# Optimization experiments

Hardware: AMD Instinct MI355X
Metric: run time of the kernel (lower is better)

Reference implementation:

```python
import jax, jax.numpy as jnp
import numpy as np

N, H, CIN, C, G = 50000, 16, 256, 256, 8
CPG = C // G          # 32 channels per group
CR = C // 4           # delta MLP hidden (delta_reduction=4)

def _lrelu(x):
    return jax.nn.leaky_relu(x, 0.1)

def setup_inputs() -> dict:
    key = jax.random.key(0)
    ks = jax.random.split(key, 16)
    def lin(k, fin, fout):
        return jax.random.normal(k, (fin, fout), jnp.float32) / np.sqrt(fin)
    return {
        'q_pts': jax.random.normal(ks[0], (N, 3), jnp.float32),
        's_pts': jax.random.normal(ks[1], (N, 3), jnp.float32),
        's_feats': jax.random.normal(ks[2], (N, CIN), jnp.float32),
        'neighb_inds': jax.random.randint(ks[3], (N, H), 0, N, jnp.int64),
        'Wq': lin(ks[4], CIN, C), 'bq': jnp.zeros((C,), jnp.float32),
        'Wk': lin(ks[5], CIN, C), 'bk': jnp.zeros((C,), jnp.float32),
        'Wv': lin(ks[6], CIN, C), 'bv': jnp.zeros((C,), jnp.float32),
        'Wd1': lin(ks[7], 3, CR), 'bd1': jnp.zeros((CR,), jnp.float32),
        'Wd2': lin(ks[8], CR, C), 'bd2': jnp.zeros((C,), jnp.float32),
        'Wa1': lin(ks[9], C, CPG), 'ba1': jnp.zeros((CPG,), jnp.float32),
        'Wa2': lin(ks[10], CPG, CPG), 'ba2': jnp.zeros((CPG,), jnp.float32),
    }

def reference(q_pts, s_pts, s_feats, neighb_inds,
              Wq, bq, Wk, bk, Wv, bv,
              Wd1, bd1, Wd2, bd2, Wa1, ba1, Wa2, ba2):
    # q/k/v projections  (N, C)
    v = s_feats @ Wv + bv
    k = s_feats @ Wk + bk
    q = s_feats @ Wq + bq
    # gather neighbor features (all indices < N, shadow mask is a no-op)
    nv = v[neighb_inds]                 # (N, H, C)
    nk = k[neighb_inds]                 # (N, H, C)
    # relative positions (torch.no_grad in source)
    rel = s_pts[neighb_inds] - q_pts[:, None, :]   # (N, H, 3)
    # delta MLP: 3 -> C/4 -> C (UnaryBlock + Linear, norm='none')
    geom = _lrelu(rel @ Wd1 + bd1) @ Wd2 + bd2     # (N, H, C)
    # geom_mode='sub': v-branch and qk-branch both subtract geom encodings
    nv = nv - geom
    # source always enters strided branch (s_pts padded before the check);
    # stride_mode='nearest' -> q feature of the first neighbor
    qf = q[neighb_inds[:, 0]]                      # (N, C)
    qk = qf[:, None, :] - nk - geom                # (N, H, C)
    # alpha MLP: NormBlock(id) + act, Linear C->CpG + act, Linear CpG->CpG
    a = _lrelu(qk)
    a = _lrelu(a @ Wa1 + ba1)
    a = a @ Wa2 + ba2                              # (N, H, CpG)
    attn = jax.nn.softmax(a, axis=1)               # softmax over neighbors
    # grouped weighted aggregation: C split as (CpG, G), attn broadcast over G
    out = (nv.reshape(N, H, CPG, G) * attn[..., None]).sum(axis=1)
    return out.reshape(N, C)
```

## Files before the change

kernel.cpp:

```cpp
#include <hip/hip_runtime.h>
#include <cstdint>
#include <cstddef>

#define N_PTS 50000
#define H 16
#define CIN 256
#define C 256
#define CPG 32
#define CR 64

typedef short bf16x8 __attribute__((ext_vector_type(8)));
typedef float f32x4 __attribute__((ext_vector_type(4)));

__device__ __forceinline__ unsigned short f2bf(float f) {
    unsigned int u = __float_as_uint(f);
    u += 0x7fff + ((u >> 16) & 1);
    return (unsigned short)(u >> 16);
}
__device__ __forceinline__ float bf2f(unsigned short s) {
    return __uint_as_float(((unsigned int)s) << 16);
}

__global__ __launch_bounds__(256) void prep_all(
    const float* __restrict__ feats,
    const float* __restrict__ Wq, const float* __restrict__ Wk,
    const float* __restrict__ Wv,
    const float* __restrict__ Wd2, const float* __restrict__ Wa1,
    const float* __restrict__ Wa2,
    unsigned short* __restrict__ A_bf16,
    unsigned short* __restrict__ gemmFrags,
    unsigned short* __restrict__ attnFrags)
{
    int bid = blockIdx.x;
    if (bid < 6250) {
        size_t i = ((size_t)bid * 256 + threadIdx.x) * 8;
        float4 f0 = *(const float4*)&feats[i];
        float4 f1 = *(const float4*)&feats[i + 4];
        unsigned short t[8] = {f2bf(f0.x), f2bf(f0.y), f2bf(f0.z), f2bf(f0.w),
                               f2bf(f1.x), f2bf(f1.y), f2bf(f1.z), f2bf(f1.w)};
        *(bf16x8*)&A_bf16[i] = *(bf16x8*)t;
    } else if (bid < 6346) {
        int t = (bid - 6250) * 256 + threadIdx.x;
        int lane = t & 63;
        int f = t >> 6;
        int ntg = f % 48;
        const float* W = ntg < 16 ? Wq : (ntg < 32 ? Wk : Wv);
        int colc = (ntg & 15) * 16 + (lane & 15);
        int row0 = (f / 48) * 32 + ((lane >> 4) << 3);
        unsigned short tmp[8];
        #pragma unroll
        for (int j = 0; j < 8; ++j) tmp[j] = f2bf(W[(size_t)(row0 + j) * 256 + colc]);
        *(bf16x8*)&gemmFrags[(size_t)t * 8] = *(bf16x8*)tmp;
    } else {
        int t = (bid - 6346) * 256 + threadIdx.x;
        if (t >= 3200) return;
        const float* W; int Nc, NT, loc, base;
        if (t < 2048)      { W = Wd2; Nc = 256; NT = 16; loc = t;        base = 0; }
        else if (t < 3072) { W = Wa1; Nc = 32;  NT = 2;  loc = t - 2048; base = 16384; }
        else               { W = Wa2; Nc = 32;  NT = 2;  loc = t - 3072; base = 24576; }
        int f = loc >> 6, lane = loc & 63;
        int kt = f / NT, nt = f - kt * NT;
        int colc = nt * 16 + (lane & 15);
        int row0 = kt * 32 + ((lane >> 4) << 3);
        unsigned short tmp[8];
        #pragma unroll
        for (int j = 0; j < 8; ++j) tmp[j] = f2bf(W[(size_t)(row0 + j) * Nc + colc]);
        *(bf16x8*)&attnFrags[(size_t)(base + loc * 8)] = *(bf16x8*)tmp;
    }
}

__global__ __launch_bounds__(256) void qkv_gemm_mfma(
    const unsigned short* __restrict__ A,
    const unsigned short* __restrict__ wfrags,
    const float* __restrict__ bq, const float* __restrict__ bk,
    const float* __restrict__ bv, unsigned short* __restrict__ out)
{
    const int tid = threadIdx.x;
    const int lane = tid & 63, wave = tid >> 6;
    const int quad = lane >> 4, col16 = lane & 15;
    const int bx = blockIdx.x, by = blockIdx.y;

    int r0 = by * 128 + wave * 32 + col16;
    int r1 = r0 + 16;
    r0 = r0 < N_PTS ? r0 : N_PTS - 1;
    r1 = r1 < N_PTS ? r1 : N_PTS - 1;
    const unsigned short* a0p = &A[(size_t)r0 * 256 + quad * 8];
    const unsigned short* a1p = &A[(size_t)r1 * 256 + quad * 8];
    const unsigned short* bp  = &wfrags[(((size_t)bx * 8) * 64 + lane) * 8];

    f32x4 acc[2][8] = {};

    #pragma unroll 2
    for (int kt = 0; kt < 8; ++kt) {
        bf16x8 af0 = *(const bf16x8*)(a0p + kt * 32);
        bf16x8 af1 = *(const bf16x8*)(a1p + kt * 32);
        const unsigned short* bkt = bp + (size_t)kt * 48 * 64 * 8;
        #pragma unroll
        for (int nt = 0; nt < 8; ++nt) {
            bf16x8 bf = *(const bf16x8*)(bkt + (size_t)nt * 64 * 8);
            acc[0][nt] = __builtin_amdgcn_mfma_f32_16x16x32_bf16(af0, bf, acc[0][nt], 0, 0, 0);
            acc[1][nt] = __builtin_amdgcn_mfma_f32_16x16x32_bf16(af1, bf, acc[1][nt], 0, 0, 0);
        }
    }

    const int mode = bx >> 1;
    const float* bias = mode == 0 ? bq : (mode == 1 ? bk : bv);
    #pragma unroll
    for (int nt = 0; nt < 8; ++nt) {
        int cIn = (bx & 1) * 128 + nt * 16 + col16;
        float bb = bias[cIn];
        int pos = mode == 0 ? cIn : (256 + 2 * cIn + (mode == 2 ? 1 : 0));
        #pragma unroll
        for (int mt = 0; mt < 2; ++mt) {
            #pragma unroll
            for (int r = 0; r < 4; ++r) {
                int row = by * 128 + wave * 32 + mt * 16 + quad * 4 + r;
                if (row < N_PTS)
                    out[(size_t)row * 768 + pos] = f2bf(acc[mt][nt][r] + bb);
            }
        }
    }
}

#define D1S 72
#define PGS 66
#define QKS 264
#define A1S 40
#define A2S 33

__global__ __launch_bounds__(256) void attn_mfma(
    const unsigned short* __restrict__ qkv,
    const float* __restrict__ q_pts, const float* __restrict__ s_pts,
    const int* __restrict__ nbr,
    const float* __restrict__ Wd1, const float* __restrict__ bd1,
    const float* __restrict__ bd2,
    const unsigned short* __restrict__ frags,
    const float* __restrict__ ba1, const float* __restrict__ ba2,
    float* __restrict__ out)
{
    __shared__ unsigned short s_d1[H * D1S];
    __shared__ float          s_pg[4 * H * PGS];
    __shared__ unsigned short s_qk[H * QKS];
    __shared__ unsigned short s_a1[H * A1S];
    __shared__ float          s_a2[H * A2S];
    __shared__ float          s_rel[4][H][3];
    __shared__ int            s_idx[4][H];

    const int tid = threadIdx.x;
    const int lane = tid & 63, wave = tid >> 6;
    const int quad = lane >> 4, col = lane & 15;
    const int n0 = blockIdx.x * 4;
    const int c = tid;

    if (tid < 64) {
        int pp = tid >> 4, hh = tid & 15;
        int idx = nbr[(size_t)(n0 + pp) * H + hh];
        s_idx[pp][hh] = idx;
        #pragma unroll
        for (int x = 0; x < 3; ++x)
            s_rel[pp][hh][x] = s_pts[(size_t)idx * 3 + x] - q_pts[(size_t)(n0 + pp) * 3 + x];
    }

    const float w1x = Wd1[lane], w1y = Wd1[64 + lane], w1z = Wd1[128 + lane];
    const float b1 = bd1[lane];
    const float b2 = bd2[c];
    bf16x8 wd2f[2][4];
    #pragma unroll
    for (int t = 0; t < 4; ++t) {
        wd2f[0][t] = *(const bf16x8*)&frags[((size_t)((0 * 16 + wave * 4 + t) * 64 + lane)) * 8];
        wd2f[1][t] = *(const bf16x8*)&frags[((size_t)((1 * 16 + wave * 4 + t) * 64 + lane)) * 8];
    }
    bf16x8 wa1f[8];
    bf16x8 wa2f = {0,0,0,0,0,0,0,0};
    if (wave < 2) {
        #pragma unroll
        for (int kt = 0; kt < 8; ++kt)
            wa1f[kt] = *(const bf16x8*)&frags[16384 + ((size_t)((kt * 2 + wave) * 64 + lane)) * 8];
        wa2f = *(const bf16x8*)&frags[24576 + ((size_t)(wave * 64 + lane)) * 8];
    }
    __syncthreads();

    float* pg = &s_pg[wave * (H * PGS)];

    for (int p = 0; p < 4; ++p) {
        const int n = n0 + p;

        #pragma unroll
        for (int pass = 0; pass < 4; ++pass) {
            int h = pass * 4 + wave;
            float v = b1 + s_rel[p][h][0] * w1x + s_rel[p][h][1] * w1y + s_rel[p][h][2] * w1z;
            s_d1[h * D1S + lane] = f2bf(fmaxf(v, 0.1f * v));
        }
        __syncthreads();

        unsigned int u[H];
        #pragma unroll
        for (int h = 0; h < H; ++h)
            u[h] = *(const unsigned int*)&qkv[(size_t)s_idx[p][h] * 768 + 256 + 2 * c];
        float qf = bf2f(qkv[(size_t)s_idx[p][0] * 768 + c]);

        {
            bf16x8 ga = *(bf16x8*)&s_d1[col * D1S + quad * 8];
            bf16x8 gb = *(bf16x8*)&s_d1[col * D1S + 32 + quad * 8];
            #pragma unroll
            for (int t = 0; t < 4; ++t) {
                f32x4 acc = {0.f, 0.f, 0.f, 0.f};
                acc = __builtin_amdgcn_mfma_f32_16x16x32_bf16(ga, wd2f[0][t], acc, 0, 0, 0);
                acc = __builtin_amdgcn_mfma_f32_16x16x32_bf16(gb, wd2f[1][t], acc, 0, 0, 0);
                #pragma unroll
                for (int rr = 0; rr < 4; ++rr)
                    pg[(quad * 4 + rr) * PGS + t * 16 + col] = acc[rr];
            }
        }

        float vg[H];
        #pragma unroll
        for (int h = 0; h < H; ++h) {
            float g = pg[h * PGS + lane] + b2;
            float nk = __uint_as_float(u[h] << 16);
            float nv = __uint_as_float(u[h] & 0xffff0000u);
            vg[h] = nv - g;
            float tq = qf - nk - g;
            s_qk[h * QKS + c] = f2bf(fmaxf(tq, 0.1f * tq));
        }
        __syncthreads();

        if (wave < 2) {
            f32x4 acc = {0.f, 0.f, 0.f, 0.f};
            #pragma unroll
            for (int kt = 0; kt < 8; ++kt) {
                bf16x8 a = *(bf16x8*)&s_qk[col * QKS + kt * 32 + quad * 8];
                acc = __builtin_amdgcn_mfma_f32_16x16x32_bf16(a, wa1f[kt], acc, 0, 0, 0);
            }
            int j = wave * 16 + col;
            float bb = ba1[j];
            #pragma unroll
            for (int rr = 0; rr < 4; ++rr) {
                float v = acc[rr] + bb;
                s_a1[(quad * 4 + rr) * A1S + j] = f2bf(fmaxf(v, 0.1f * v));
            }
        }
        __syncthreads();

        if (wave < 2) {
            bf16x8 aa = *(bf16x8*)&s_a1[col * A1S + quad * 8];
            f32x4 acc = {0.f, 0.f, 0.f, 0.f};
            acc = __builtin_amdgcn_mfma_f32_16x16x32_bf16(aa, wa2f, acc, 0, 0, 0);
            int j = wave * 16 + col;
            float bb = ba2[j];
            #pragma unroll
            for (int rr = 0; rr < 4; ++rr)
                s_a2[(quad * 4 + rr) * A2S + j] = acc[rr] + bb;
        }
        __syncthreads();

        if (wave == 0) {
            int j = lane & 31, hb = (lane >> 5) * 8;
            float vals[8];
            float mx = -1e30f;
            #pragma unroll
            for (int i = 0; i < 8; ++i) {
                vals[i] = s_a2[(hb + i) * A2S + j];
                mx = fmaxf(mx, vals[i]);
            }
            mx = fmaxf(mx, __shfl_xor(mx, 32));
            float sum = 0.f;
            #pragma unroll
            for (int i = 0; i < 8; ++i) { vals[i] = __expf(vals[i] - mx); sum += vals[i]; }
            sum += __shfl_xor(sum, 32);
            float inv = 1.f / sum;
            #pragma unroll
            for (int i = 0; i < 8; ++i) s_a2[(hb + i) * A2S + j] = vals[i] * inv;
        }
        __syncthreads();

        float o = 0.f;
        const int aj = c >> 3;
        #pragma unroll
        for (int h = 0; h < H; ++h) o += vg[h] * s_a2[h * A2S + aj];
        out[(size_t)n * C + c] = o;
    }
}


extern "C" void kernel_launch(void* const* d_in, const int* in_sizes, int n_in,
                              void* d_out, int out_size, void* d_ws, size_t ws_size,
                              hipStream_t stream) {
    const float* q_pts   = (const float*)d_in[0];
    const float* s_pts   = (const float*)d_in[1];
    const float* s_feats = (const float*)d_in[2];
    const int*   nbr     = (const int*)d_in[3];
    const float* Wq  = (const float*)d_in[4];
    const float* bq  = (const float*)d_in[5];
    const float* Wk  = (const float*)d_in[6];
    const float* bk  = (const float*)d_in[7];
    const float* Wv  = (const float*)d_in[8];
    const float* bv  = (const float*)d_in[9];
    const float* Wd1 = (const float*)d_in[10];
    const float* bd1 = (const float*)d_in[11];
    const float* Wd2 = (const float*)d_in[12];
    const float* bd2 = (const float*)d_in[13];
    const float* Wa1 = (const float*)d_in[14];
    const float* ba1 = (const float*)d_in[15];
    const float* Wa2 = (const float*)d_in[16];
    const float* ba2 = (const float*)d_in[17];

    float* out = (float*)d_out;
    char* ws = (char*)d_ws;
    unsigned short* A_bf16    = (unsigned short*)(ws);
    unsigned short* qkvb      = (unsigned short*)(ws + 25600000);
    unsigned short* attnFrags = (unsigned short*)(ws + 102400000);
    unsigned short* gemmFrags = (unsigned short*)(ws + 102451200);

    prep_all<<<6359, 256, 0, stream>>>(s_feats, Wq, Wk, Wv, Wd2, Wa1, Wa2,
                                       A_bf16, gemmFrags, attnFrags);

    dim3 g1(6, (N_PTS + 127) / 128);
    qkv_gemm_mfma<<<g1, 256, 0, stream>>>(A_bf16, gemmFrags, bq, bk, bv, qkvb);

    attn_mfma<<<(N_PTS / 4), 256, 0, stream>>>(qkvb, q_pts, s_pts, nbr,
                                               Wd1, bd1, bd2, attnFrags,
                                               ba1, ba2, out);
}
```

Before: 414.4 us.

## Process two points per iteration so all waves share alpha MLP work

The attention kernel now handles 8 points per block and pairs them per loop iteration. The delta MLP and qk stages are computed for two points with double-buffered shared arrays. All four waves then run the alpha MLP MFMAs (two waves per point) and two waves run the softmax, where previously only two waves or one wave were active. The number of barriers per point is halved, at the cost of higher register pressure from holding vg0 and vg1, extra shared memory, and fewer blocks in the grid.

Result: no change. 419.5 us (+1.2%).

```diff
diff --git a/kernel.cpp b/kernel.cpp
--- a/kernel.cpp
+++ b/kernel.cpp
@@ -127,6 +127,7 @@
 #define QKS 264
 #define A1S 40
 #define A2S 33
+#define PPB 8
 
 __global__ __launch_bounds__(256) void attn_mfma(
     const unsigned short* __restrict__ qkv,
@@ -138,21 +139,23 @@
     const float* __restrict__ ba1, const float* __restrict__ ba2,
     float* __restrict__ out)
 {
-    __shared__ unsigned short s_d1[H * D1S];
+    __shared__ unsigned short s_d1[2][H * D1S];
     __shared__ float          s_pg[4 * H * PGS];
-    __shared__ unsigned short s_qk[H * QKS];
-    __shared__ unsigned short s_a1[H * A1S];
-    __shared__ float          s_a2[H * A2S];
-    __shared__ float          s_rel[4][H][3];
-    __shared__ int            s_idx[4][H];
+    __shared__ unsigned short s_qk[2][H * QKS];
+    __shared__ unsigned short s_a1[2][H * A1S];
+    __shared__ float          s_a2[2][H * A2S];
+    __shared__ float          s_rel[PPB][H][3];
+    __shared__ int            s_idx[PPB][H];
 
     const int tid = threadIdx.x;
     const int lane = tid & 63, wave = tid >> 6;
     const int quad = lane >> 4, col = lane & 15;
-    const int n0 = blockIdx.x * 4;
+    const int pw = wave >> 1;
+    const int hx = wave & 1;
+    const int n0 = blockIdx.x * PPB;
     const int c = tid;
 
-    if (tid < 64) {
+    if (tid < PPB * H) {
         int pp = tid >> 4, hh = tid & 15;
         int idx = nbr[(size_t)(n0 + pp) * H + hh];
         s_idx[pp][hh] = idx;
@@ -171,37 +174,40 @@
         wd2f[1][t] = *(const bf16x8*)&frags[((size_t)((1 * 16 + wave * 4 + t) * 64 + lane)) * 8];
     }
     bf16x8 wa1f[8];
-    bf16x8 wa2f = {0,0,0,0,0,0,0,0};
-    if (wave < 2) {
-        #pragma unroll
-        for (int kt = 0; kt < 8; ++kt)
-            wa1f[kt] = *(const bf16x8*)&frags[16384 + ((size_t)((kt * 2 + wave) * 64 + lane)) * 8];
-        wa2f = *(const bf16x8*)&frags[24576 + ((size_t)(wave * 64 + lane)) * 8];
-    }
+    #pragma unroll
+    for (int kt = 0; kt < 8; ++kt)
+        wa1f[kt] = *(const bf16x8*)&frags[16384 + ((size_t)((kt * 2 + hx) * 64 + lane)) * 8];
+    bf16x8 wa2f = *(const bf16x8*)&frags[24576 + ((size_t)(hx * 64 + lane)) * 8];
     __syncthreads();
 
     float* pg = &s_pg[wave * (H * PGS)];
 
-    for (int p = 0; p < 4; ++p) {
-        const int n = n0 + p;
-
-        #pragma unroll
-        for (int pass = 0; pass < 4; ++pass) {
-            int h = pass * 4 + wave;
-            float v = b1 + s_rel[p][h][0] * w1x + s_rel[p][h][1] * w1y + s_rel[p][h][2] * w1z;
-            s_d1[h * D1S + lane] = f2bf(fmaxf(v, 0.1f * v));
-        }
-        __syncthreads();
-
-        unsigned int u[H];
-        #pragma unroll
-        for (int h = 0; h < H; ++h)
-            u[h] = *(const unsigned int*)&qkv[(size_t)s_idx[p][h] * 768 + 256 + 2 * c];
-        float qf = bf2f(qkv[(size_t)s_idx[p][0] * 768 + c]);
+    for (int pr = 0; pr < PPB / 2; ++pr) {
+        const int p0 = 2 * pr, p1 = 2 * pr + 1;
+
+        #pragma unroll
+        for (int pt = 0; pt < 2; ++pt) {
+            #pragma unroll
+            for (int pass = 0; pass < 4; ++pass) {
+                int h = pass * 4 + wave;
+                const float* rel = s_rel[p0 + pt][h];
+                float v = b1 + rel[0] * w1x + rel[1] * w1y + rel[2] * w1z;
+                s_d1[pt][h * D1S + lane] = f2bf(fmaxf(v, 0.1f * v));
+            }
+        }
+        __syncthreads();
+
+        float vg0[H], vg1[H];
 
         {
-            bf16x8 ga = *(bf16x8*)&s_d1[col * D1S + quad * 8];
-            bf16x8 gb = *(bf16x8*)&s_d1[col * D1S + 32 + quad * 8];
+            unsigned int u[H];
+            #pragma unroll
+            for (int h = 0; h < H; ++h)
+                u[h] = *(const unsigned int*)&qkv[(size_t)s_idx[p0][h] * 768 + 256 + 2 * c];
+            float qf = bf2f(qkv[(size_t)s_idx[p0][0] * 768 + c]);
+
+            bf16x8 ga = *(bf16x8*)&s_d1[0][col * D1S + quad * 8];
+            bf16x8 gb = *(bf16x8*)&s_d1[0][col * D1S + 32 + quad * 8];
             #pragma unroll
             for (int t = 0; t < 4; ++t) {
                 f32x4 acc = {0.f, 0.f, 0.f, 0.f};
@@ -211,56 +217,83 @@
                 for (int rr = 0; rr < 4; ++rr)
                     pg[(quad * 4 + rr) * PGS + t * 16 + col] = acc[rr];
             }
-        }
-
-        float vg[H];
-        #pragma unroll
-        for (int h = 0; h < H; ++h) {
-            float g = pg[h * PGS + lane] + b2;
-            float nk = __uint_as_float(u[h] << 16);
-            float nv = __uint_as_float(u[h] & 0xffff0000u);
-            vg[h] = nv - g;
-            float tq = qf - nk - g;
-            s_qk[h * QKS + c] = f2bf(fmaxf(tq, 0.1f * tq));
-        }
-        __syncthreads();
-
-        if (wave < 2) {
+            #pragma unroll
+            for (int h = 0; h < H; ++h) {
+                float g = pg[h * PGS + lane] + b2;
+                float nk = __uint_as_float(u[h] << 16);
+                float nv = __uint_as_float(u[h] & 0xffff0000u);
+                vg0[h] = nv - g;
+                float tq = qf - nk - g;
+                s_qk[0][h * QKS + c] = f2bf(fmaxf(tq, 0.1f * tq));
+            }
+        }
+        {
+            unsigned int u[H];
+            #pragma unroll
+            for (int h = 0; h < H; ++h)
+                u[h] = *(const unsigned int*)&qkv[(size_t)s_idx[p1][h] * 768 + 256 + 2 * c];
+            float qf = bf2f(qkv[(size_t)s_idx[p1][0] * 768 + c]);
+
+            bf16x8 ga = *(bf16x8*)&s_d1[1][col * D1S + quad * 8];
+            bf16x8 gb = *(bf16x8*)&s_d1[1][col * D1S + 32 + quad * 8];
+            #pragma unroll
+            for (int t = 0; t < 4; ++t) {
+                f32x4 acc = {0.f, 0.f, 0.f, 0.f};
+                acc = __builtin_amdgcn_mfma_f32_16x16x32_bf16(ga, wd2f[0][t], acc, 0, 0, 0);
+                acc = __builtin_amdgcn_mfma_f32_16x16x32_bf16(gb, wd2f[1][t], acc, 0, 0, 0);
+                #pragma unroll
+                for (int rr = 0; rr < 4; ++rr)
+                    pg[(quad * 4 + rr) * PGS + t * 16 + col] = acc[rr];
+            }
+            #pragma unroll
+            for (int h = 0; h < H; ++h) {
+                float g = pg[h * PGS + lane] + b2;
+                float nk = __uint_as_float(u[h] << 16);
+                float nv = __uint_as_float(u[h] & 0xffff0000u);
+                vg1[h] = nv - g;
+                float tq = qf - nk - g;
+                s_qk[1][h * QKS + c] = f2bf(fmaxf(tq, 0.1f * tq));
+            }
+        }
+        __syncthreads();
+
+        {
             f32x4 acc = {0.f, 0.f, 0.f, 0.f};
             #pragma unroll
             for (int kt = 0; kt < 8; ++kt) {
-                bf16x8 a = *(bf16x8*)&s_qk[col * QKS + kt * 32 + quad * 8];
+                bf16x8 a = *(bf16x8*)&s_qk[pw][col * QKS + kt * 32 + quad * 8];
                 acc = __builtin_amdgcn_mfma_f32_16x16x32_bf16(a, wa1f[kt], acc, 0, 0, 0);
             }
-            int j = wave * 16 + col;
+            int j = hx * 16 + col;
             float bb = ba1[j];
             #pragma unroll
             for (int rr = 0; rr < 4; ++rr) {
                 float v = acc[rr] + bb;
-                s_a1[(quad * 4 + rr) * A1S + j] = f2bf(fmaxf(v, 0.1f * v));
-            }
-        }
-        __syncthreads();
-
-        if (wave < 2) {
-            bf16x8 aa = *(bf16x8*)&s_a1[col * A1S + quad * 8];
+                s_a1[pw][(quad * 4 + rr) * A1S + j] = f2bf(fmaxf(v, 0.1f * v));
+            }
+        }
+        __syncthreads();
+
+        {
+            bf16x8 aa = *(bf16x8*)&s_a1[pw][col * A1S + quad * 8];
             f32x4 acc = {0.f, 0.f, 0.f, 0.f};
             acc = __builtin_amdgcn_mfma_f32_16x16x32_bf16(aa, wa2f, acc, 0, 0, 0);
-            int j = wave * 16 + col;
+            int j = hx * 16 + col;
             float bb = ba2[j];
             #pragma unroll
             for (int rr = 0; rr < 4; ++rr)
-                s_a2[(quad * 4 + rr) * A2S + j] = acc[rr] + bb;
-        }
-        __syncthreads();
-
-        if (wave == 0) {
+                s_a2[pw][(quad * 4 + rr) * A2S + j] = acc[rr] + bb;
+        }
+        __syncthreads();
+
+        if (wave < 2) {
+            float* a2b = s_a2[wave];
             int j = lane & 31, hb = (lane >> 5) * 8;
             float vals[8];
             float mx = -1e30f;
             #pragma unroll
             for (int i = 0; i < 8; ++i) {
-                vals[i] = s_a2[(hb + i) * A2S + j];
+                vals[i] = a2b[(hb + i) * A2S + j];
                 mx = fmaxf(mx, vals[i]);
             }
             mx = fmaxf(mx, __shfl_xor(mx, 32));
@@ -270,15 +303,19 @@
             sum += __shfl_xor(sum, 32);
             float inv = 1.f / sum;
             #pragma unroll
-            for (int i = 0; i < 8; ++i) s_a2[(hb + i) * A2S + j] = vals[i] * inv;
-        }
-        __syncthreads();
-
-        float o = 0.f;
+            for (int i = 0; i < 8; ++i) a2b[(hb + i) * A2S + j] = vals[i] * inv;
+        }
+        __syncthreads();
+
+        float o0 = 0.f, o1 = 0.f;
         const int aj = c >> 3;
         #pragma unroll
-        for (int h = 0; h < H; ++h) o += vg[h] * s_a2[h * A2S + aj];
-        out[(size_t)n * C + c] = o;
+        for (int h = 0; h < H; ++h) {
+            o0 += vg0[h] * s_a2[0][h * A2S + aj];
+            o1 += vg1[h] * s_a2[1][h * A2S + aj];
+        }
+        out[(size_t)(n0 + p0) * C + c] = o0;
+        out[(size_t)(n0 + p1) * C + c] = o1;
     }
 }
 
@@ -318,7 +355,7 @@
     dim3 g1(6, (N_PTS + 127) / 128);
     qkv_gemm_mfma<<<g1, 256, 0, stream>>>(A_bf16, gemmFrags, bq, bk, bv, qkvb);
 
-    attn_mfma<<<(N_PTS / 4), 256, 0, stream>>>(qkvb, q_pts, s_pts, nbr,
-                                               Wd1, bd1, bd2, attnFrags,
-                                               ba1, ba2, out);
-}
+    attn_mfma<<<(N_PTS / PPB), 256, 0, stream>>>(qkvb, q_pts, s_pts, nbr,
+                                                 Wd1, bd1, bd2, attnFrags,
+                                                 ba1, ba2, out);
+}
```
